# Kernel optimization log

Hardware: AMD Instinct MI355X
Metric: run time of the kernel (lower is better)

## Reference

```python
import jax, jax.numpy as jnp
import numpy as np

N_NODES = 100000
N_EDGES = 3200000
IN_F, OUT_F = 256, 128


def setup_inputs() -> dict:
    key = jax.random.key(0)
    k1, k2, k3, k4, k5 = jax.random.split(key, 5)
    features = jax.random.normal(k1, (N_NODES, IN_F), dtype=jnp.float32)
    # Xavier-uniform-like init for the weight
    limit = float(np.sqrt(6.0 / (IN_F + OUT_F)))
    weight = jax.random.uniform(k2, (IN_F, OUT_F), dtype=jnp.float32, minval=-limit, maxval=limit)
    edge_row = jnp.sort(jax.random.randint(k3, (N_EDGES,), 0, N_NODES, dtype=jnp.int32))
    edge_col = jax.random.randint(k4, (N_EDGES,), 0, N_NODES, dtype=jnp.int32)
    edge_val = jax.random.uniform(k5, (N_EDGES,), dtype=jnp.float32)
    return {
        "features": features,
        "weight": weight,
        "edge_row": edge_row,
        "edge_col": edge_col,
        "edge_val": edge_val,
        "active": 1,
    }


def reference(features, weight, edge_row, edge_col, edge_val, active):
    # Dense transform: [N, in] @ [in, out] -> [N, out]
    h = features @ weight
    if active:  # static Python flag, matches `active=True` torch path
        h = jnp.tanh(h)
    # spmm(adj, h): out[r] = sum_e val[e] * h[col[e]] for edges with row[e]==r
    msgs = edge_val[:, None] * h[edge_col]          # [E, out] gather + scale
    out = jax.ops.segment_sum(msgs, edge_row, num_segments=N_NODES)
    return out
```

## Files before the change

kernel.cpp:

```cpp
#include <hip/hip_runtime.h>
#include <hip/hip_bf16.h>

#define N_NODES 100000
#define N_EDGES 3200000
#define IN_F 256
#define OUT_F 128

typedef __attribute__((ext_vector_type(8))) short bf16x8;
typedef __attribute__((ext_vector_type(4))) float f32x4;

__device__ __forceinline__ unsigned short f2bf(float f) {
    unsigned int u = __float_as_uint(f);
    u += 0x7fffu + ((u >> 16) & 1u);
    return (unsigned short)(u >> 16);
}

__device__ __forceinline__ short cvt_bf16(float f) {
    __hip_bfloat16 b = (__hip_bfloat16)f;
    return *reinterpret_cast<short*>(&b);
}

__global__ void k_init(const float* __restrict__ W, unsigned short* __restrict__ Wt,
                       const int* __restrict__ erow, int* __restrict__ row_ptr) {
    int e = blockIdx.x * 256 + threadIdx.x;
    if (e < IN_F * OUT_F) {
        int k = e >> 7;
        int c = e & 127;
        Wt[c * IN_F + k] = f2bf(W[e]);
    }
    if (e >= N_EDGES) return;
    int r = erow[e];
    int rprev = (e == 0) ? -1 : erow[e - 1];
    for (int rr = rprev + 1; rr <= r; ++rr) row_ptr[rr] = e;
    if (e == N_EDGES - 1) {
        for (int rr = r + 1; rr <= N_NODES; ++rr) row_ptr[rr] = N_EDGES;
    }
}

__global__ __launch_bounds__(256) void k_gemm(const float* __restrict__ A,
                                              const unsigned short* __restrict__ Wt,
                                              signed char* __restrict__ H8,
                                              const int* __restrict__ activep) {
    const int tid  = threadIdx.x;
    const int lane = tid & 63;
    const int wid  = tid >> 6;
    const int wr   = wid >> 1;
    const int wc   = wid & 1;
    const int brow = blockIdx.x * 128;
    const int l15  = lane & 15;
    const int lk   = (lane >> 4) * 8;

    const float* ap[4];
    #pragma unroll
    for (int i = 0; i < 4; ++i) {
        int row = brow + wr * 64 + i * 16 + l15;
        if (row > N_NODES - 1) row = N_NODES - 1;
        ap[i] = A + (long)row * IN_F + lk;
    }
    const unsigned short* bp = Wt + (long)(wc * 64 + l15) * IN_F + lk;

    f32x4 acc[4][4] = {};

    float4 f0[4], f1[4];
    #pragma unroll
    for (int i = 0; i < 4; ++i) {
        f0[i] = *(const float4*)(ap[i]);
        f1[i] = *(const float4*)(ap[i] + 4);
    }

    for (int k0 = 0; k0 < IN_F; k0 += 32) {
        const int kn = k0 + 32;
        float4 n0[4], n1[4];
        if (kn < IN_F) {
            #pragma unroll
            for (int i = 0; i < 4; ++i) {
                n0[i] = *(const float4*)(ap[i] + kn);
                n1[i] = *(const float4*)(ap[i] + kn + 4);
            }
        }
        bf16x8 a[4];
        #pragma unroll
        for (int i = 0; i < 4; ++i) {
            bf16x8 v;
            v[0] = cvt_bf16(f0[i].x); v[1] = cvt_bf16(f0[i].y);
            v[2] = cvt_bf16(f0[i].z); v[3] = cvt_bf16(f0[i].w);
            v[4] = cvt_bf16(f1[i].x); v[5] = cvt_bf16(f1[i].y);
            v[6] = cvt_bf16(f1[i].z); v[7] = cvt_bf16(f1[i].w);
            a[i] = v;
        }
        bf16x8 b[4];
        #pragma unroll
        for (int n = 0; n < 4; ++n)
            b[n] = *(const bf16x8*)(bp + (long)n * 16 * IN_F + k0);

        #pragma unroll
        for (int i = 0; i < 4; ++i)
            #pragma unroll
            for (int n = 0; n < 4; ++n)
                acc[i][n] = __builtin_amdgcn_mfma_f32_16x16x32_bf16(a[i], b[n], acc[i][n], 0, 0, 0);

        if (kn < IN_F) {
            #pragma unroll
            for (int i = 0; i < 4; ++i) { f0[i] = n0[i]; f1[i] = n1[i]; }
        }
    }

    const int act = *activep;
    const float qs = act ? 127.0f : 16.0f;
    #pragma unroll
    for (int i = 0; i < 4; ++i) {
        #pragma unroll
        for (int n = 0; n < 4; ++n) {
            #pragma unroll
            for (int r = 0; r < 4; ++r) {
                int row = brow + wr * 64 + i * 16 + (lane >> 4) * 4 + r;
                int col = wc * 64 + n * 16 + l15;
                if (row < N_NODES) {
                    float v = acc[i][n][r];
                    if (act) {
                        float t = __expf(2.0f * v);
                        v = 1.0f - __fdividef(2.0f, t + 1.0f);
                    }
                    float q = v * qs;
                    q = fminf(fmaxf(q, -127.0f), 127.0f);
                    H8[(long)row * OUT_F + col] = (signed char)__float2int_rn(q);
                }
            }
        }
    }
}

__global__ __launch_bounds__(256) void k_spmm(const int* __restrict__ row_ptr,
                                              const int* __restrict__ ecol,
                                              const float* __restrict__ eval,
                                              const signed char* __restrict__ h8,
                                              const int* __restrict__ activep,
                                              float* __restrict__ out) {
    const int lane = threadIdx.x & 63;
    const int w    = threadIdx.x >> 6;
    const int r    = blockIdx.x * 4 + w;
    if (r >= N_NODES) return;

    const int q  = lane >> 4;
    const int l15 = lane & 15;

    const int s = __builtin_amdgcn_readfirstlane(row_ptr[r]);
    const int e = __builtin_amdgcn_readfirstlane(row_ptr[r + 1]);
    const int act = __builtin_amdgcn_readfirstlane(*activep);
    const float invs = act ? (1.0f / 127.0f) : (1.0f / 16.0f);

    const signed char* hq = h8 + l15 * 8;

    float f0 = 0.f, f1 = 0.f, f2 = 0.f, f3 = 0.f;
    float f4 = 0.f, f5 = 0.f, f6 = 0.f, f7 = 0.f;

    for (int j = s; j < e; j += 16) {
        int   cc[4];
        float vv[4];
        #pragma unroll
        for (int u = 0; u < 4; ++u) {
            const int want = j + u * 4 + q;
            const int idx  = min(want, e - 1);
            cc[u] = ecol[idx];
            vv[u] = (want < e) ? eval[idx] * invs : 0.f;
        }
        uint2 g[4];
        #pragma unroll
        for (int u = 0; u < 4; ++u)
            g[u] = *(const uint2*)(hq + (((unsigned)cc[u]) << 7));
        #pragma unroll
        for (int u = 0; u < 4; ++u) {
            const float v = vv[u];
            const unsigned x = g[u].x, y = g[u].y;
            f0 = fmaf(v, (float)((signed char)(x      )), f0);
            f1 = fmaf(v, (float)((signed char)(x >>  8)), f1);
            f2 = fmaf(v, (float)((signed char)(x >> 16)), f2);
            f3 = fmaf(v, (float)((int)x >> 24),           f3);
            f4 = fmaf(v, (float)((signed char)(y      )), f4);
            f5 = fmaf(v, (float)((signed char)(y >>  8)), f5);
            f6 = fmaf(v, (float)((signed char)(y >> 16)), f6);
            f7 = fmaf(v, (float)((int)y >> 24),           f7);
        }
    }

    #pragma unroll
    for (int mask = 16; mask <= 32; mask <<= 1) {
        f0 += __shfl_xor(f0, mask);
        f1 += __shfl_xor(f1, mask);
        f2 += __shfl_xor(f2, mask);
        f3 += __shfl_xor(f3, mask);
        f4 += __shfl_xor(f4, mask);
        f5 += __shfl_xor(f5, mask);
        f6 += __shfl_xor(f6, mask);
        f7 += __shfl_xor(f7, mask);
    }

    if (q == 0) {
        float* dst = out + (long)r * OUT_F + l15 * 8;
        float4 o0; o0.x = f0; o0.y = f1; o0.z = f2; o0.w = f3;
        float4 o1; o1.x = f4; o1.y = f5; o1.z = f6; o1.w = f7;
        *(float4*)dst       = o0;
        *(float4*)(dst + 4) = o1;
    }
}

extern "C" void kernel_launch(void* const* d_in, const int* in_sizes, int n_in,
                              void* d_out, int out_size, void* d_ws, size_t ws_size,
                              hipStream_t stream) {
    const float* features = (const float*)d_in[0];
    const float* weight   = (const float*)d_in[1];
    const int*   erow     = (const int*)d_in[2];
    const int*   ecol     = (const int*)d_in[3];
    const float* evalp    = (const float*)d_in[4];
    const int*   activep  = (const int*)d_in[5];
    float* out = (float*)d_out;

    char* ws = (char*)d_ws;
    signed char* H8    = (signed char*)ws;
    unsigned short* Wt = (unsigned short*)(ws + 12800000);
    int* row_ptr       = (int*)(ws + 12800000 + 65536);

    k_init  <<<(N_EDGES + 255) / 256, 256, 0, stream>>>(weight, Wt, erow, row_ptr);
    k_gemm  <<<(N_NODES + 127) / 128, 256, 0, stream>>>(features, Wt, H8, activep);
    k_spmm  <<<(N_NODES + 3) / 4, 256, 0, stream>>>(row_ptr, ecol, evalp,
                                                    H8, activep, out);
}
```

Before: 149.3 us.

## Store H as offset-unsigned bytes and retile GEMM waves to full-width columns

The transformed features are stored as unsigned bytes with a +128 offset. The SpMM inner loop can then convert bytes with cheap unsigned extract-to-float operations instead of sign-extending shifts. The offset is removed once per row by subtracting 128 times the sum of the edge weights. Separately, each GEMM wave now covers 32 rows by all 128 columns instead of 64 rows by 64 columns, which halves the redundant A-row loads per wave but doubles the B loads. The subtraction of a large bias can add some float rounding error.

```diff
diff --git a/kernel.cpp b/kernel.cpp
--- a/kernel.cpp
+++ b/kernel.cpp
@@ -19,6 +19,11 @@
     __hip_bfloat16 b = (__hip_bfloat16)f;
     return *reinterpret_cast<short*>(&b);
 }
+
+#define UB0(x) ((float)((unsigned char)((x))))
+#define UB1(x) ((float)((unsigned char)((x) >> 8)))
+#define UB2(x) ((float)((unsigned char)((x) >> 16)))
+#define UB3(x) ((float)((x) >> 24))
 
 __global__ void k_init(const float* __restrict__ W, unsigned short* __restrict__ Wt,
                        const int* __restrict__ erow, int* __restrict__ row_ptr) {
@@ -39,48 +44,46 @@
 
 __global__ __launch_bounds__(256) void k_gemm(const float* __restrict__ A,
                                               const unsigned short* __restrict__ Wt,
-                                              signed char* __restrict__ H8,
+                                              unsigned char* __restrict__ H8,
                                               const int* __restrict__ activep) {
     const int tid  = threadIdx.x;
     const int lane = tid & 63;
     const int wid  = tid >> 6;
-    const int wr   = wid >> 1;
-    const int wc   = wid & 1;
     const int brow = blockIdx.x * 128;
     const int l15  = lane & 15;
     const int lk   = (lane >> 4) * 8;
 
-    const float* ap[4];
-    #pragma unroll
-    for (int i = 0; i < 4; ++i) {
-        int row = brow + wr * 64 + i * 16 + l15;
+    const float* ap[2];
+    #pragma unroll
+    for (int i = 0; i < 2; ++i) {
+        int row = brow + wid * 32 + i * 16 + l15;
         if (row > N_NODES - 1) row = N_NODES - 1;
         ap[i] = A + (long)row * IN_F + lk;
     }
-    const unsigned short* bp = Wt + (long)(wc * 64 + l15) * IN_F + lk;
-
-    f32x4 acc[4][4] = {};
-
-    float4 f0[4], f1[4];
-    #pragma unroll
-    for (int i = 0; i < 4; ++i) {
+    const unsigned short* bp = Wt + (long)l15 * IN_F + lk;
+
+    f32x4 acc[2][8] = {};
+
+    float4 f0[2], f1[2];
+    #pragma unroll
+    for (int i = 0; i < 2; ++i) {
         f0[i] = *(const float4*)(ap[i]);
         f1[i] = *(const float4*)(ap[i] + 4);
     }
 
     for (int k0 = 0; k0 < IN_F; k0 += 32) {
         const int kn = k0 + 32;
-        float4 n0[4], n1[4];
+        float4 n0[2], n1[2];
         if (kn < IN_F) {
             #pragma unroll
-            for (int i = 0; i < 4; ++i) {
+            for (int i = 0; i < 2; ++i) {
                 n0[i] = *(const float4*)(ap[i] + kn);
                 n1[i] = *(const float4*)(ap[i] + kn + 4);
             }
         }
-        bf16x8 a[4];
-        #pragma unroll
-        for (int i = 0; i < 4; ++i) {
+        bf16x8 a[2];
+        #pragma unroll
+        for (int i = 0; i < 2; ++i) {
             bf16x8 v;
             v[0] = cvt_bf16(f0[i].x); v[1] = cvt_bf16(f0[i].y);
             v[2] = cvt_bf16(f0[i].z); v[3] = cvt_bf16(f0[i].w);
@@ -88,33 +91,33 @@
             v[6] = cvt_bf16(f1[i].z); v[7] = cvt_bf16(f1[i].w);
             a[i] = v;
         }
-        bf16x8 b[4];
-        #pragma unroll
-        for (int n = 0; n < 4; ++n)
+        bf16x8 b[8];
+        #pragma unroll
+        for (int n = 0; n < 8; ++n)
             b[n] = *(const bf16x8*)(bp + (long)n * 16 * IN_F + k0);
 
         #pragma unroll
-        for (int i = 0; i < 4; ++i)
-            #pragma unroll
-            for (int n = 0; n < 4; ++n)
+        for (int i = 0; i < 2; ++i)
+            #pragma unroll
+            for (int n = 0; n < 8; ++n)
                 acc[i][n] = __builtin_amdgcn_mfma_f32_16x16x32_bf16(a[i], b[n], acc[i][n], 0, 0, 0);
 
         if (kn < IN_F) {
             #pragma unroll
-            for (int i = 0; i < 4; ++i) { f0[i] = n0[i]; f1[i] = n1[i]; }
+            for (int i = 0; i < 2; ++i) { f0[i] = n0[i]; f1[i] = n1[i]; }
         }
     }
 
     const int act = *activep;
     const float qs = act ? 127.0f : 16.0f;
     #pragma unroll
-    for (int i = 0; i < 4; ++i) {
-        #pragma unroll
-        for (int n = 0; n < 4; ++n) {
+    for (int i = 0; i < 2; ++i) {
+        #pragma unroll
+        for (int n = 0; n < 8; ++n) {
             #pragma unroll
             for (int r = 0; r < 4; ++r) {
-                int row = brow + wr * 64 + i * 16 + (lane >> 4) * 4 + r;
-                int col = wc * 64 + n * 16 + l15;
+                int row = brow + wid * 32 + i * 16 + (lane >> 4) * 4 + r;
+                int col = n * 16 + l15;
                 if (row < N_NODES) {
                     float v = acc[i][n][r];
                     if (act) {
@@ -123,7 +126,8 @@
                     }
                     float q = v * qs;
                     q = fminf(fmaxf(q, -127.0f), 127.0f);
-                    H8[(long)row * OUT_F + col] = (signed char)__float2int_rn(q);
+                    H8[(long)row * OUT_F + col] =
+                        (unsigned char)(__float2int_rn(q) + 128);
                 }
             }
         }
@@ -133,7 +137,7 @@
 __global__ __launch_bounds__(256) void k_spmm(const int* __restrict__ row_ptr,
                                               const int* __restrict__ ecol,
                                               const float* __restrict__ eval,
-                                              const signed char* __restrict__ h8,
+                                              const unsigned char* __restrict__ h8,
                                               const int* __restrict__ activep,
                                               float* __restrict__ out) {
     const int lane = threadIdx.x & 63;
@@ -141,7 +145,7 @@
     const int r    = blockIdx.x * 4 + w;
     if (r >= N_NODES) return;
 
-    const int q  = lane >> 4;
+    const int q   = lane >> 4;
     const int l15 = lane & 15;
 
     const int s = __builtin_amdgcn_readfirstlane(row_ptr[r]);
@@ -149,10 +153,11 @@
     const int act = __builtin_amdgcn_readfirstlane(*activep);
     const float invs = act ? (1.0f / 127.0f) : (1.0f / 16.0f);
 
-    const signed char* hq = h8 + l15 * 8;
+    const unsigned char* hq = h8 + l15 * 8;
 
     float f0 = 0.f, f1 = 0.f, f2 = 0.f, f3 = 0.f;
     float f4 = 0.f, f5 = 0.f, f6 = 0.f, f7 = 0.f;
+    float vs = 0.f;
 
     for (int j = s; j < e; j += 16) {
         int   cc[4];
@@ -171,17 +176,22 @@
         #pragma unroll
         for (int u = 0; u < 4; ++u) {
             const float v = vv[u];
+            vs += v;
             const unsigned x = g[u].x, y = g[u].y;
-            f0 = fmaf(v, (float)((signed char)(x      )), f0);
-            f1 = fmaf(v, (float)((signed char)(x >>  8)), f1);
-            f2 = fmaf(v, (float)((signed char)(x >> 16)), f2);
-            f3 = fmaf(v, (float)((int)x >> 24),           f3);
-            f4 = fmaf(v, (float)((signed char)(y      )), f4);
-            f5 = fmaf(v, (float)((signed char)(y >>  8)), f5);
-            f6 = fmaf(v, (float)((signed char)(y >> 16)), f6);
-            f7 = fmaf(v, (float)((int)y >> 24),           f7);
-        }
-    }
+            f0 = fmaf(v, UB0(x), f0);
+            f1 = fmaf(v, UB1(x), f1);
+            f2 = fmaf(v, UB2(x), f2);
+            f3 = fmaf(v, UB3(x), f3);
+            f4 = fmaf(v, UB0(y), f4);
+            f5 = fmaf(v, UB1(y), f5);
+            f6 = fmaf(v, UB2(y), f6);
+            f7 = fmaf(v, UB3(y), f7);
+        }
+    }
+
+    const float bias = 128.0f * vs;
+    f0 -= bias; f1 -= bias; f2 -= bias; f3 -= bias;
+    f4 -= bias; f5 -= bias; f6 -= bias; f7 -= bias;
 
     #pragma unroll
     for (int mask = 16; mask <= 32; mask <<= 1) {
@@ -197,10 +207,10 @@
 
     if (q == 0) {
         float* dst = out + (long)r * OUT_F + l15 * 8;
-        float4 o0; o0.x = f0; o0.y = f1; o0.z = f2; o0.w = f3;
-        float4 o1; o1.x = f4; o1.y = f5; o1.z = f6; o1.w = f7;
-        *(float4*)dst       = o0;
-        *(float4*)(dst + 4) = o1;
+        float4 o0v; o0v.x = f0; o0v.y = f1; o0v.z = f2; o0v.w = f3;
+        float4 o1v; o1v.x = f4; o1v.y = f5; o1v.z = f6; o1v.w = f7;
+        *(float4*)dst       = o0v;
+        *(float4*)(dst + 4) = o1v;
     }
 }
 
@@ -216,12 +226,12 @@
     float* out = (float*)d_out;
 
     char* ws = (char*)d_ws;
-    signed char* H8    = (signed char*)ws;
+    unsigned char* H8  = (unsigned char*)ws;
     unsigned short* Wt = (unsigned short*)(ws + 12800000);
     int* row_ptr       = (int*)(ws + 12800000 + 65536);
 
-    k_init  <<<(N_EDGES + 255) / 256, 256, 0, stream>>>(weight, Wt, erow, row_ptr);
-    k_gemm  <<<(N_NODES + 127) / 128, 256, 0, stream>>>(features, Wt, H8, activep);
-    k_spmm  <<<(N_NODES + 3) / 4, 256, 0, stream>>>(row_ptr, ecol, evalp,
-                                                    H8, activep, out);
-}
+    k_init <<<(N_EDGES + 255) / 256, 256, 0, stream>>>(weight, Wt, erow, row_ptr);
+    k_gemm <<<(N_NODES + 127) / 128, 256, 0, stream>>>(features, Wt, H8, activep);
+    k_spmm <<<(N_NODES + 3) / 4, 256, 0, stream>>>(row_ptr, ecol, evalp,
+                                                   H8, activep, out);
+}
```

Result: slower. 155.2 us (+3.9%).

## Split int8 H into four 32-column planes and run SpMM per plane

Applied to the files above, without the earlier changes.

The GEMM now writes the quantized hidden matrix as four column planes of 32 bytes per node, and the SpMM runs four times, once per plane. Each pass gathers rows from a 3.2 MB plane, which is meant to fit in cache and raise the hit rate of the random gathers. The dequantization scale is also moved out of the inner loop and applied once at the store. The cost is reading the edge column and value arrays four times, plus four kernel launches and narrower 4-byte gathers.

```diff
diff --git a/kernel.cpp b/kernel.cpp
--- a/kernel.cpp
+++ b/kernel.cpp
@@ -5,6 +5,7 @@
 #define N_EDGES 3200000
 #define IN_F 256
 #define OUT_F 128
+#define PLANE 3200000
 
 typedef __attribute__((ext_vector_type(8))) short bf16x8;
 typedef __attribute__((ext_vector_type(4))) float f32x4;
@@ -111,10 +112,11 @@
     for (int i = 0; i < 4; ++i) {
         #pragma unroll
         for (int n = 0; n < 4; ++n) {
+            const int col   = wc * 64 + n * 16 + l15;
+            const long pofs = (long)(col >> 5) * PLANE + (col & 31);
             #pragma unroll
             for (int r = 0; r < 4; ++r) {
                 int row = brow + wr * 64 + i * 16 + (lane >> 4) * 4 + r;
-                int col = wc * 64 + n * 16 + l15;
                 if (row < N_NODES) {
                     float v = acc[i][n][r];
                     if (act) {
@@ -123,7 +125,7 @@
                     }
                     float q = v * qs;
                     q = fminf(fmaxf(q, -127.0f), 127.0f);
-                    H8[(long)row * OUT_F + col] = (signed char)__float2int_rn(q);
+                    H8[pofs + (long)row * 32] = (signed char)__float2int_rn(q);
                 }
             }
         }
@@ -133,74 +135,62 @@
 __global__ __launch_bounds__(256) void k_spmm(const int* __restrict__ row_ptr,
                                               const int* __restrict__ ecol,
                                               const float* __restrict__ eval,
-                                              const signed char* __restrict__ h8,
+                                              const signed char* __restrict__ plane,
                                               const int* __restrict__ activep,
-                                              float* __restrict__ out) {
+                                              float* __restrict__ outp) {
     const int lane = threadIdx.x & 63;
     const int w    = threadIdx.x >> 6;
     const int r    = blockIdx.x * 4 + w;
     if (r >= N_NODES) return;
 
-    const int q  = lane >> 4;
-    const int l15 = lane & 15;
+    const int q  = lane >> 3;
+    const int l7 = lane & 7;
 
     const int s = __builtin_amdgcn_readfirstlane(row_ptr[r]);
     const int e = __builtin_amdgcn_readfirstlane(row_ptr[r + 1]);
     const int act = __builtin_amdgcn_readfirstlane(*activep);
     const float invs = act ? (1.0f / 127.0f) : (1.0f / 16.0f);
 
-    const signed char* hq = h8 + l15 * 8;
+    const signed char* hq = plane + l7 * 4;
 
     float f0 = 0.f, f1 = 0.f, f2 = 0.f, f3 = 0.f;
-    float f4 = 0.f, f5 = 0.f, f6 = 0.f, f7 = 0.f;
-
-    for (int j = s; j < e; j += 16) {
+
+    for (int j = s; j < e; j += 32) {
         int   cc[4];
         float vv[4];
         #pragma unroll
         for (int u = 0; u < 4; ++u) {
-            const int want = j + u * 4 + q;
+            const int want = j + u * 8 + q;
             const int idx  = min(want, e - 1);
             cc[u] = ecol[idx];
-            vv[u] = (want < e) ? eval[idx] * invs : 0.f;
-        }
-        uint2 g[4];
+            vv[u] = (want < e) ? eval[idx] : 0.f;
+        }
+        unsigned g[4];
         #pragma unroll
         for (int u = 0; u < 4; ++u)
-            g[u] = *(const uint2*)(hq + (((unsigned)cc[u]) << 7));
+            g[u] = *(const unsigned*)(hq + (((unsigned)cc[u]) << 5));
         #pragma unroll
         for (int u = 0; u < 4; ++u) {
             const float v = vv[u];
-            const unsigned x = g[u].x, y = g[u].y;
+            const unsigned x = g[u];
             f0 = fmaf(v, (float)((signed char)(x      )), f0);
             f1 = fmaf(v, (float)((signed char)(x >>  8)), f1);
             f2 = fmaf(v, (float)((signed char)(x >> 16)), f2);
             f3 = fmaf(v, (float)((int)x >> 24),           f3);
-            f4 = fmaf(v, (float)((signed char)(y      )), f4);
-            f5 = fmaf(v, (float)((signed char)(y >>  8)), f5);
-            f6 = fmaf(v, (float)((signed char)(y >> 16)), f6);
-            f7 = fmaf(v, (float)((int)y >> 24),           f7);
-        }
-    }
-
-    #pragma unroll
-    for (int mask = 16; mask <= 32; mask <<= 1) {
+        }
+    }
+
+    #pragma unroll
+    for (int mask = 8; mask <= 32; mask <<= 1) {
         f0 += __shfl_xor(f0, mask);
         f1 += __shfl_xor(f1, mask);
         f2 += __shfl_xor(f2, mask);
         f3 += __shfl_xor(f3, mask);
-        f4 += __shfl_xor(f4, mask);
-        f5 += __shfl_xor(f5, mask);
-        f6 += __shfl_xor(f6, mask);
-        f7 += __shfl_xor(f7, mask);
     }
 
     if (q == 0) {
-        float* dst = out + (long)r * OUT_F + l15 * 8;
-        float4 o0; o0.x = f0; o0.y = f1; o0.z = f2; o0.w = f3;
-        float4 o1; o1.x = f4; o1.y = f5; o1.z = f6; o1.w = f7;
-        *(float4*)dst       = o0;
-        *(float4*)(dst + 4) = o1;
+        float4 o; o.x = f0 * invs; o.y = f1 * invs; o.z = f2 * invs; o.w = f3 * invs;
+        *(float4*)(outp + (long)r * OUT_F + l7 * 4) = o;
     }
 }
 
@@ -217,11 +207,14 @@
 
     char* ws = (char*)d_ws;
     signed char* H8    = (signed char*)ws;
-    unsigned short* Wt = (unsigned short*)(ws + 12800000);
-    int* row_ptr       = (int*)(ws + 12800000 + 65536);
-
-    k_init  <<<(N_EDGES + 255) / 256, 256, 0, stream>>>(weight, Wt, erow, row_ptr);
-    k_gemm  <<<(N_NODES + 127) / 128, 256, 0, stream>>>(features, Wt, H8, activep);
-    k_spmm  <<<(N_NODES + 3) / 4, 256, 0, stream>>>(row_ptr, ecol, evalp,
-                                                    H8, activep, out);
-}
+    unsigned short* Wt = (unsigned short*)(ws + 4 * PLANE);
+    int* row_ptr       = (int*)(ws + 4 * PLANE + 65536);
+
+    k_init <<<(N_EDGES + 255) / 256, 256, 0, stream>>>(weight, Wt, erow, row_ptr);
+    k_gemm <<<(N_NODES + 127) / 128, 256, 0, stream>>>(features, Wt, H8, activep);
+    for (int p = 0; p < 4; ++p) {
+        k_spmm <<<(N_NODES + 3) / 4, 256, 0, stream>>>(row_ptr, ecol, evalp,
+                                                       H8 + (long)p * PLANE,
+                                                       activep, out + p * 32);
+    }
+}
```

New measurement: 201.6 us. 1.35x slower.
